# Optimization experiments

Measured on AMD Instinct MI355X. Metric: run time of the kernel, lower is better.

## Reference

```python
import jax, jax.numpy as jnp
import numpy as np

B, T, H, K, C, U, IN = 128, 800, 512, 10, 80, 64, 3


def setup_inputs() -> dict:
    key = jax.random.key(0)
    ks = jax.random.split(key, 6)
    s = 0.08  # small init so exp() window params stay stable
    return {
        "strokes": jax.random.normal(ks[0], (B, T, IN), jnp.float32),
        "sentences": jax.random.randint(ks[1], (B, U), 0, C),
        "sentences_mask": jnp.ones((B, U), jnp.float32),
        "W_ih": jax.random.normal(ks[2], (4 * H, IN + C), jnp.float32) * s,
        "W_hh": jax.random.normal(ks[3], (4 * H, H), jnp.float32) * s,
        "b_ih": jnp.zeros((4 * H,), jnp.float32),
        "b_hh": jnp.zeros((4 * H,), jnp.float32),
        "W_win": jax.random.normal(ks[4], (3 * K, H), jnp.float32) * s,
        "b_win": jnp.zeros((3 * K,), jnp.float32),
    }


def reference(strokes, sentences, sentences_mask, W_ih, W_hh, b_ih, b_hh, W_win, b_win):
    # Pre-mask the one-hot character encoding: [B, U, C]
    onehot = jax.nn.one_hot(sentences, C, dtype=jnp.float32) * sentences_mask[:, :, None]
    u = jnp.arange(U, dtype=jnp.float32)  # character position grid
    bias = b_ih + b_hh

    def step(carry, x_t):
        h, c, kappa_prev, window = carry
        inp = jnp.concatenate([x_t, window], axis=-1)           # [B, IN+C]
        gates = inp @ W_ih.T + h @ W_hh.T + bias                 # [B, 4H]
        i, f, g, o = jnp.split(gates, 4, axis=-1)                # torch LSTMCell order i,f,g,o
        i, f, o = jax.nn.sigmoid(i), jax.nn.sigmoid(f), jax.nn.sigmoid(o)
        c = f * c + i * jnp.tanh(g)
        h = o * jnp.tanh(c)
        # Gaussian window parameters (eq. 48-51 in Graves 2013)
        p = h @ W_win.T + b_win                                  # [B, 3K]
        a_hat, b_hat, k_hat = jnp.split(p, 3, axis=-1)
        alpha = jnp.exp(a_hat)
        beta = jnp.exp(b_hat)
        kappa = kappa_prev + jnp.exp(k_hat)
        # phi[b,u] = sum_k alpha * exp(-beta * (kappa - u)^2)
        d = kappa[:, :, None] - u[None, None, :]                 # [B, K, U]
        phi = jnp.sum(alpha[:, :, None] * jnp.exp(-beta[:, :, None] * d * d), axis=1)  # [B, U]
        window = jnp.einsum('bu,buc->bc', phi, onehot)           # [B, C]
        return (h, c, kappa, window), (h, window, phi)

    init = (
        jnp.zeros((B, H), jnp.float32),
        jnp.zeros((B, H), jnp.float32),
        jnp.zeros((B, K), jnp.float32),
        jnp.zeros((B, C), jnp.float32),
    )
    xs = jnp.swapaxes(strokes, 0, 1)                             # [T, B, IN]
    _, (h_seq, w_seq, phi_seq) = jax.lax.scan(step, init, xs)
    return (
        jnp.swapaxes(h_seq, 0, 1),    # [B, T, H]
        jnp.swapaxes(w_seq, 0, 1),    # [B, T, C]
        jnp.swapaxes(phi_seq, 0, 1),  # [B, T, U]
    )
```

## Files before the change

### kernel.cpp

```cpp
#include <hip/hip_runtime.h>
#include <hip/hip_bf16.h>
#include <math.h>

#define B_   128
#define T_   800
#define H_   512
#define K_   10
#define C_   80
#define U_   64
#define IN_  3

#define NG   4
#define BPG  64
#define BT   32
#define NT   256
#define KROW 608

#define WS_GPP_F (2*B_*KROW)
#define WS_BAR_F (WS_GPP_F + NG*BPG*BT*30)
#define WS_TOTAL_F (WS_BAR_F + NG*8*32)

#define OFF_H    0ull
#define OFF_W    ((size_t)B_ * T_ * H_)
#define OFF_PHI  (OFF_W + (size_t)B_ * T_ * C_)

typedef __attribute__((ext_vector_type(8))) short short8;
typedef __attribute__((ext_vector_type(4))) float f32x4;

#define SWZB(row)    (((row) ^ ((row) >> 2)) & 3)
#define SWIDX(row,k) ((row)*KROW + ((((k) >> 3) ^ SWZB(row)) << 3) + ((k) & 7))
#define LDFRAG(arr,row,u) (*(const short8*)&(arr)[(row)*KROW + (((u) ^ SWZB(row)) << 3)])

__device__ __forceinline__ void stb_f32(float* p, float v) {
  asm volatile("global_store_dword %0, %1, off sc0 sc1" :: "v"(p), "v"(v) : "memory");
}
__device__ __forceinline__ void stb_u32(unsigned* p, unsigned v) {
  asm volatile("global_store_dword %0, %1, off sc0 sc1" :: "v"(p), "v"(v) : "memory");
}
__device__ __forceinline__ void fence_vm() {
  asm volatile("s_waitcnt vmcnt(0)" ::: "memory");
}
__device__ __forceinline__ void flag_add(unsigned* p) {
  __hip_atomic_fetch_add(p, 1u, __ATOMIC_RELAXED, __HIP_MEMORY_SCOPE_AGENT);
}
__device__ __forceinline__ unsigned flag_sum(unsigned* base, int nlines) {
  unsigned s = 0;
  for (int i = 0; i < nlines; ++i)
    s += __hip_atomic_load(base + i * 32, __ATOMIC_RELAXED, __HIP_MEMORY_SCOPE_AGENT);
  return s;
}
__device__ __forceinline__ void acq_fence(unsigned* p) {
  (void)__hip_atomic_load(p, __ATOMIC_ACQUIRE, __HIP_MEMORY_SCOPE_AGENT);
}
__device__ __forceinline__ float sigmoidf_(float v) { return 1.0f / (1.0f + expf(-v)); }
__device__ __forceinline__ unsigned pack_hl(float v) {
  unsigned hb = __float_as_uint(v) >> 16;
  float rs = v - __uint_as_float(hb << 16);
  unsigned lb = __float_as_uint(rs) >> 16;
  return (hb << 16) | lb;
}

__global__ void __launch_bounds__(256, 2)
init_ws_kernel(float* __restrict__ ws) {
  size_t i = (size_t)blockIdx.x * 256 + threadIdx.x;
  const size_t n = (size_t)WS_TOTAL_F;
  const size_t stride = (size_t)gridDim.x * 256;
  for (; i < n; i += stride) ws[i] = 0.0f;
}

__global__ void __launch_bounds__(NT, 1)
graves_kernel(const float* __restrict__ x,
              const int*   __restrict__ sent,
              const float* __restrict__ smask,
              const float* __restrict__ W_ih,
              const float* __restrict__ W_hh,
              const float* __restrict__ b_ih,
              const float* __restrict__ b_hh,
              const float* __restrict__ W_win,
              const float* __restrict__ b_win,
              float* __restrict__ out,
              float* __restrict__ ws)
{
  const int tid = threadIdx.x;
  const int bid = blockIdx.x;
  const int g   = bid >> 6;
  const int ub  = bid & (BPG - 1);
  const int b0  = g * BT;
  const int u0  = ub * 8;

  unsigned* gbufu = (unsigned*)ws;
  float*    gpp   = ws + WS_GPP_F;
  unsigned* fb    = (unsigned*)(ws + WS_BAR_F) + (size_t)g * 256;
  unsigned* c1l   = fb;
  unsigned* c2l   = fb + 4 * 32;

  __shared__ __align__(16) short whi[32 * KROW];
  __shared__ __align__(16) short wlo[32 * KROW];
  __shared__ __align__(16) short shi[32 * KROW];
  __shared__ __align__(16) short slo[32 * KROW];
  __shared__ __align__(16) float glf[1024];
  __shared__ float hT[8 * 32];
  __shared__ float wwin[8 * 30];
  __shared__ float xwb[32 * 4];
  __shared__ int   sentl[U_];
  __shared__ float maskl[U_];
  __shared__ float kapl[K_ + 6];

  float* pred  = glf;
  float* pl    = glf + 256;
  float* abkA  = glf + 288;
  float* abkB  = glf + 304;
  float* abkK  = glf + 320;
  float* phim  = glf + 336;

  for (int idx = tid; idx < 32 * KROW; idx += NT) {
    const int r = idx / KROW, k = idx - r * KROW;
    const int uu = r >> 2, gate = r & 3, gr = gate * H_ + u0 + uu;
    float wv = 0.0f;
    if (k < H_)      wv = W_hh[(size_t)gr * H_ + k];
    else if (k < H_ + C_) wv = W_ih[(size_t)gr * (IN_ + C_) + IN_ + (k - H_)];
    const unsigned hb = __float_as_uint(wv) >> 16;
    const float rs = wv - __uint_as_float(hb << 16);
    const unsigned lb = __float_as_uint(rs) >> 16;
    const int li = SWIDX(r, k);
    whi[li] = (short)hb;
    wlo[li] = (short)lb;
  }
  for (int idx = tid; idx < 32 * 16; idx += NT) {
    const int b2 = idx >> 4, k = (H_ + C_) + (idx & 15);
    shi[SWIDX(b2, k)] = 0; slo[SWIDX(b2, k)] = 0;
  }
  if (tid < 32) {
    const int uu = tid >> 2, gate = tid & 3, gr = gate * H_ + u0 + uu;
    xwb[tid * 4 + 0] = W_ih[(size_t)gr * (IN_ + C_) + 0];
    xwb[tid * 4 + 1] = W_ih[(size_t)gr * (IN_ + C_) + 1];
    xwb[tid * 4 + 2] = W_ih[(size_t)gr * (IN_ + C_) + 2];
    xwb[tid * 4 + 3] = b_ih[gr] + b_hh[gr];
  }
  for (int idx = tid; idx < 240; idx += NT) {
    const int uu = idx / 30, j = idx - uu * 30;
    wwin[idx] = W_win[(size_t)j * H_ + u0 + uu];
  }
  const bool isWB = (ub < BT);
  const int  wb_b = b0 + ub;
  if (isWB) {
    if (tid < U_) { sentl[tid] = sent[wb_b * U_ + tid]; maskl[tid] = smask[wb_b * U_ + tid]; }
    if (tid < K_) kapl[tid] = 0.0f;
  }
  __syncthreads();

  const int lane = tid & 63;
  const int wid  = tid >> 6;
  const int ni   = wid & 1;
  const int kh   = wid >> 1;
  const int r16  = lane & 15;
  const int g4   = lane >> 4;
  const int bb   = ni * 16 + r16;

  float cr0 = 0.0f, cr1 = 0.0f;

#define GSTEP(ks) { \
    const int uu_ = (ks) * 4 + g4; \
    const short8 bh = LDFRAG(shi, bb, uu_); \
    const short8 bl = LDFRAG(slo, bb, uu_); \
    const short8 ah0 = LDFRAG(whi, r16, uu_); \
    const short8 al0 = LDFRAG(wlo, r16, uu_); \
    const short8 ah1 = LDFRAG(whi, 16 + r16, uu_); \
    const short8 al1 = LDFRAG(wlo, 16 + r16, uu_); \
    a0 = __builtin_amdgcn_mfma_f32_16x16x32_bf16(ah0, bh, a0, 0, 0, 0); \
    a0 = __builtin_amdgcn_mfma_f32_16x16x32_bf16(ah0, bl, a0, 0, 0, 0); \
    a0 = __builtin_amdgcn_mfma_f32_16x16x32_bf16(al0, bh, a0, 0, 0, 0); \
    a1 = __builtin_amdgcn_mfma_f32_16x16x32_bf16(ah1, bh, a1, 0, 0, 0); \
    a1 = __builtin_amdgcn_mfma_f32_16x16x32_bf16(ah1, bl, a1, 0, 0, 0); \
    a1 = __builtin_amdgcn_mfma_f32_16x16x32_bf16(al1, bh, a1, 0, 0, 0); \
  }

  for (int t = 0; t <= T_; ++t) {
    if (!isWB && t == T_) break;

    const unsigned* pIn  = gbufu + (size_t)((t & 1) ^ 1) * (B_ * KROW);
    unsigned*       pInW = gbufu + (size_t)((t & 1) ^ 1) * (B_ * KROW);
    unsigned*       pOut = gbufu + (size_t)(t & 1) * (B_ * KROW);

    if (tid == 0 && t > 0) {
      const unsigned tgt = 64u * (unsigned)t;
      while (flag_sum(c1l, 4) < tgt) __builtin_amdgcn_s_sleep(1);
      acq_fence(c1l);
    }
    __syncthreads();

    float xv0 = 0.f, xv1 = 0.f, xv2 = 0.f;
    float pv0=0,pv1=0,pv2=0,pv3=0,pv4=0,pv5=0,pv6=0,pv7=0;
    if (t < T_) {
      const int sb = tid & 31, seg = tid >> 5;
      const unsigned* grow = pIn + (size_t)(b0 + sb) * KROW + seg * 64;
      uint4 v[16];
      #pragma unroll
      for (int i = 0; i < 16; ++i) v[i] = *(const uint4*)(grow + i * 4);
      #pragma unroll
      for (int i = 0; i < 16; ++i) {
        const int k = seg * 64 + i * 4;
        const int idx = SWIDX(sb, k);
        const unsigned h01 = (v[i].x >> 16) | ((v[i].y >> 16) << 16);
        const unsigned h23 = (v[i].z >> 16) | ((v[i].w >> 16) << 16);
        const unsigned l01 = (v[i].x & 0xffffu) | ((v[i].y & 0xffffu) << 16);
        const unsigned l23 = (v[i].z & 0xffffu) | ((v[i].w & 0xffffu) << 16);
        *(uint2*)&shi[idx] = make_uint2(h01, h23);
        *(uint2*)&slo[idx] = make_uint2(l01, l23);
      }
      if (kh == 0) {
        const float* xp = x + ((size_t)(b0 + bb) * T_ + t) * IN_;
        xv0 = xp[0]; xv1 = xp[1]; xv2 = xp[2];
      }
    }
    if (isWB && t >= 1 && tid < 240) {
      const int j = tid % 30, ch = tid / 30;
      const float* gp = gpp + (((size_t)(g * BPG + ch * 8) * BT + ub) * 30 + j);
      pv0 = gp[0*BT*30]; pv1 = gp[1*BT*30]; pv2 = gp[2*BT*30]; pv3 = gp[3*BT*30];
      pv4 = gp[4*BT*30]; pv5 = gp[5*BT*30]; pv6 = gp[6*BT*30]; pv7 = gp[7*BT*30];
    }
    __syncthreads();

    if (isWB && t >= 1) {
      if (tid < 240) pred[tid] = ((pv0+pv1)+(pv2+pv3))+((pv4+pv5)+(pv6+pv7));
      __syncthreads();
      if (tid < 30) {
        float s = b_win[tid];
        #pragma unroll
        for (int ch = 0; ch < 8; ++ch) s += pred[ch * 30 + tid];
        pl[tid] = s;
      }
      __syncthreads();
      if (tid < K_) {
        abkA[tid] = expf(pl[tid]);
        abkB[tid] = expf(pl[K_ + tid]);
        const float kv = kapl[tid] + expf(pl[2 * K_ + tid]);
        kapl[tid] = kv;
        abkK[tid] = kv;
      }
      __syncthreads();
      if (tid < U_) {
        const float fu = (float)tid;
        float s = 0.0f;
        #pragma unroll
        for (int j2 = 0; j2 < K_; ++j2) {
          const float d = abkK[j2] - fu;
          s = fmaf(abkA[j2], expf(-abkB[j2] * d * d), s);
        }
        phim[tid] = s * maskl[tid];
        out[OFF_PHI + ((size_t)wb_b * T_ + (t - 1)) * U_ + tid] = s;
      }
      __syncthreads();
      if (tid < C_) {
        float wv = 0.0f;
        #pragma unroll
        for (int u = 0; u < U_; ++u) wv += (sentl[u] == tid) ? phim[u] : 0.0f;
        stb_u32(&pInW[(size_t)wb_b * KROW + H_ + tid], pack_hl(wv));
        out[OFF_W + ((size_t)wb_b * T_ + (t - 1)) * C_ + tid] = wv;
      }
      fence_vm();
      __syncthreads();
      if (tid == 0) flag_add(c2l + (ub & 1) * 32);
    }
    if (t == T_) break;

    f32x4 a0 = {0.f, 0.f, 0.f, 0.f}, a1 = {0.f, 0.f, 0.f, 0.f};
    for (int ks = kh * 8; ks < kh * 8 + 8; ++ks) GSTEP(ks);

    if (tid == 0 && t > 0) {
      const unsigned tgt = 32u * (unsigned)t;
      while (flag_sum(c2l, 2) < tgt) __builtin_amdgcn_s_sleep(1);
      acq_fence(c2l);
    }
    __syncthreads();

    {
      const int sb = tid & 31, seg = tid >> 5;
      #pragma unroll
      for (int i = 0; i < 10; ++i) {
        const int c = seg * 10 + i;
        const unsigned v = pIn[(size_t)(b0 + sb) * KROW + H_ + c];
        const int idx = SWIDX(sb, H_ + c);
        shi[idx] = (short)(v >> 16);
        slo[idx] = (short)(v & 0xffffu);
      }
    }
    __syncthreads();

    if (kh == 0) { GSTEP(16); }
    else         { GSTEP(17); GSTEP(18); }

    if (kh == 1) {
      #pragma unroll
      for (int e = 0; e < 4; ++e) {
        glf[(ni * 2 + 0) * 256 + (g4 * 4 + e) * 16 + r16] = a0[e];
        glf[(ni * 2 + 1) * 256 + (g4 * 4 + e) * 16 + r16] = a1[e];
      }
    }
    __syncthreads();
    if (kh == 0) {
      #pragma unroll
      for (int mi = 0; mi < 2; ++mi) {
        float ge[4];
        #pragma unroll
        for (int e = 0; e < 4; ++e) {
          const int r = mi * 16 + g4 * 4 + e;
          const float av = ((mi == 0) ? a0[e] : a1[e]) + glf[(ni * 2 + mi) * 256 + (g4 * 4 + e) * 16 + r16];
          ge[e] = av + xwb[r*4+0]*xv0 + xwb[r*4+1]*xv1 + xwb[r*4+2]*xv2 + xwb[r*4+3];
        }
        const float iv = sigmoidf_(ge[0]);
        const float fv = sigmoidf_(ge[1]);
        const float gv = tanhf(ge[2]);
        const float ov = sigmoidf_(ge[3]);
        const float cprev = (mi == 0) ? cr0 : cr1;
        const float cv = fmaf(fv, cprev, iv * gv);
        if (mi == 0) cr0 = cv; else cr1 = cv;
        const float hv = ov * tanhf(cv);
        const int uu = mi * 4 + g4;
        hT[uu * 32 + bb] = hv;
        stb_u32(&pOut[(size_t)(b0 + bb) * KROW + (u0 + uu)], pack_hl(hv));
        out[OFF_H + ((size_t)(b0 + bb) * T_ + t) * H_ + (u0 + uu)] = hv;
      }
    }
    __syncthreads();

    for (int it = tid; it < BT * 30; it += NT) {
      const int b2 = it / 30, j = it - b2 * 30;
      float s = 0.0f;
      #pragma unroll
      for (int uu = 0; uu < 8; ++uu) s = fmaf(wwin[uu * 30 + j], hT[uu * 32 + b2], s);
      stb_f32(&gpp[((size_t)bid * BT + b2) * 30 + j], s);
    }
    fence_vm();
    __syncthreads();
    if (tid == 0) flag_add(c1l + (ub & 3) * 32);
  }
#undef GSTEP
}

extern "C" void kernel_launch(void* const* d_in, const int* in_sizes, int n_in,
                              void* d_out, int out_size, void* d_ws, size_t ws_size,
                              hipStream_t stream) {
  const float* x     = (const float*)d_in[0];
  const int*   sent  = (const int*)  d_in[1];
  const float* smask = (const float*)d_in[2];
  const float* W_ih  = (const float*)d_in[3];
  const float* W_hh  = (const float*)d_in[4];
  const float* b_ih  = (const float*)d_in[5];
  const float* b_hh  = (const float*)d_in[6];
  const float* W_win = (const float*)d_in[7];
  const float* b_win = (const float*)d_in[8];
  float* ws  = (float*)d_ws;
  float* out = (float*)d_out;

  hipLaunchKernelGGL(init_ws_kernel, dim3(512), dim3(256), 0, stream, ws);
  hipLaunchKernelGGL(graves_kernel, dim3(NG * BPG), dim3(NT), 0, stream,
                     x, sent, smask, W_ih, W_hh, b_ih, b_hh, W_win, b_win, out, ws);
}
```

Baseline: 10.54 ms.

## Replace two-barrier window stage with atomic fixed-point accumulation and redundant per-block window compute

Instead of writer blocks gathering per-block window-projection partials and publishing the window vector behind a second grid barrier, every block atomically adds fixed-point deltas of its partial projection into a shared 64-bit accumulator. Every block then recomputes alpha, beta, kappa, phi and the window for its whole batch group locally in shared memory. This removes the second cross-block barrier and the window round trip through global memory each timestep. The cost is redundant exp work in all blocks, 64-bit atomics with fixed-point quantisation (up to about 2^-32 per partial), and __expf approximations, so results may differ slightly from before.

```diff
diff --git a/kernel.cpp b/kernel.cpp
--- a/kernel.cpp
+++ b/kernel.cpp
@@ -15,9 +15,10 @@
 #define BT   32
 #define NT   256
 #define KROW 608
-
-#define WS_GPP_F (2*B_*KROW)
-#define WS_BAR_F (WS_GPP_F + NG*BPG*BT*30)
+#define HB   512
+
+#define WS_PACC_F  (2*B_*HB)
+#define WS_BAR_F   (WS_PACC_F + NG*BT*30*2)
 #define WS_TOTAL_F (WS_BAR_F + NG*8*32)
 
 #define OFF_H    0ull
@@ -31,9 +32,6 @@
 #define SWIDX(row,k) ((row)*KROW + ((((k) >> 3) ^ SWZB(row)) << 3) + ((k) & 7))
 #define LDFRAG(arr,row,u) (*(const short8*)&(arr)[(row)*KROW + (((u) ^ SWZB(row)) << 3)])
 
-__device__ __forceinline__ void stb_f32(float* p, float v) {
-  asm volatile("global_store_dword %0, %1, off sc0 sc1" :: "v"(p), "v"(v) : "memory");
-}
 __device__ __forceinline__ void stb_u32(unsigned* p, unsigned v) {
   asm volatile("global_store_dword %0, %1, off sc0 sc1" :: "v"(p), "v"(v) : "memory");
 }
@@ -43,11 +41,8 @@
 __device__ __forceinline__ void flag_add(unsigned* p) {
   __hip_atomic_fetch_add(p, 1u, __ATOMIC_RELAXED, __HIP_MEMORY_SCOPE_AGENT);
 }
-__device__ __forceinline__ unsigned flag_sum(unsigned* base, int nlines) {
-  unsigned s = 0;
-  for (int i = 0; i < nlines; ++i)
-    s += __hip_atomic_load(base + i * 32, __ATOMIC_RELAXED, __HIP_MEMORY_SCOPE_AGENT);
-  return s;
+__device__ __forceinline__ unsigned flag_ld(unsigned* p) {
+  return __hip_atomic_load(p, __ATOMIC_RELAXED, __HIP_MEMORY_SCOPE_AGENT);
 }
 __device__ __forceinline__ void acq_fence(unsigned* p) {
   (void)__hip_atomic_load(p, __ATOMIC_ACQUIRE, __HIP_MEMORY_SCOPE_AGENT);
@@ -58,6 +53,10 @@
   float rs = v - __uint_as_float(hb << 16);
   unsigned lb = __float_as_uint(rs) >> 16;
   return (hb << 16) | lb;
+}
+__device__ __forceinline__ float comb_hl(short h, short l) {
+  return __uint_as_float((unsigned)(unsigned short)h << 16) +
+         __uint_as_float((unsigned)(unsigned short)l << 16);
 }
 
 __global__ void __launch_bounds__(256, 2)
@@ -88,36 +87,26 @@
   const int b0  = g * BT;
   const int u0  = ub * 8;
 
-  unsigned* gbufu = (unsigned*)ws;
-  float*    gpp   = ws + WS_GPP_F;
-  unsigned* fb    = (unsigned*)(ws + WS_BAR_F) + (size_t)g * 256;
-  unsigned* c1l   = fb;
-  unsigned* c2l   = fb + 4 * 32;
+  unsigned*  gbuf   = (unsigned*)ws;
+  long long* pacc_g = (long long*)(ws + WS_PACC_F) + (size_t)g * (BT * 30);
+  unsigned*  fb     = (unsigned*)(ws + WS_BAR_F) + (size_t)g * 256;
+  unsigned*  c1l    = fb;
 
   __shared__ __align__(16) short whi[32 * KROW];
   __shared__ __align__(16) short wlo[32 * KROW];
   __shared__ __align__(16) short shi[32 * KROW];
   __shared__ __align__(16) short slo[32 * KROW];
-  __shared__ __align__(16) float glf[1024];
+  __shared__ float pbufS[32][32];
   __shared__ float hT[8 * 32];
   __shared__ float wwin[8 * 30];
   __shared__ float xwb[32 * 4];
-  __shared__ int   sentl[U_];
-  __shared__ float maskl[U_];
-  __shared__ float kapl[K_ + 6];
-
-  float* pred  = glf;
-  float* pl    = glf + 256;
-  float* abkA  = glf + 288;
-  float* abkB  = glf + 304;
-  float* abkK  = glf + 320;
-  float* phim  = glf + 336;
+  float* pbf = &pbufS[0][0];
 
   for (int idx = tid; idx < 32 * KROW; idx += NT) {
     const int r = idx / KROW, k = idx - r * KROW;
     const int uu = r >> 2, gate = r & 3, gr = gate * H_ + u0 + uu;
     float wv = 0.0f;
-    if (k < H_)      wv = W_hh[(size_t)gr * H_ + k];
+    if (k < H_)           wv = W_hh[(size_t)gr * H_ + k];
     else if (k < H_ + C_) wv = W_ih[(size_t)gr * (IN_ + C_) + IN_ + (k - H_)];
     const unsigned hb = __float_as_uint(wv) >> 16;
     const float rs = wv - __uint_as_float(hb << 16);
@@ -141,13 +130,6 @@
     const int uu = idx / 30, j = idx - uu * 30;
     wwin[idx] = W_win[(size_t)j * H_ + u0 + uu];
   }
-  const bool isWB = (ub < BT);
-  const int  wb_b = b0 + ub;
-  if (isWB) {
-    if (tid < U_) { sentl[tid] = sent[wb_b * U_ + tid]; maskl[tid] = smask[wb_b * U_ + tid]; }
-    if (tid < K_) kapl[tid] = 0.0f;
-  }
-  __syncthreads();
 
   const int lane = tid & 63;
   const int wid  = tid >> 6;
@@ -157,7 +139,20 @@
   const int g4   = lane >> 4;
   const int bb   = ni * 16 + r16;
 
+  const int pb = tid >> 3, ug = tid & 7;
+  float msk[8]; int snt[8];
+  #pragma unroll
+  for (int i = 0; i < 8; ++i) {
+    msk[i] = smask[(size_t)(b0 + pb) * U_ + ug * 8 + i];
+    snt[i] = sent [(size_t)(b0 + pb) * U_ + ug * 8 + i];
+  }
+  const bool isWriter = (ub < BT);
+  const int  wb_b = b0 + ub;
+  __syncthreads();
+
   float cr0 = 0.0f, cr1 = 0.0f;
+  long long prevp[4] = {0, 0, 0, 0};
+  float kprevf[4] = {0.f, 0.f, 0.f, 0.f};
 
 #define GSTEP(ks) { \
     const int uu_ = (ks) * 4 + g4; \
@@ -176,24 +171,23 @@
   }
 
   for (int t = 0; t <= T_; ++t) {
-    if (!isWB && t == T_) break;
-
-    const unsigned* pIn  = gbufu + (size_t)((t & 1) ^ 1) * (B_ * KROW);
-    unsigned*       pInW = gbufu + (size_t)((t & 1) ^ 1) * (B_ * KROW);
-    unsigned*       pOut = gbufu + (size_t)(t & 1) * (B_ * KROW);
-
-    if (tid == 0 && t > 0) {
-      const unsigned tgt = 64u * (unsigned)t;
-      while (flag_sum(c1l, 4) < tgt) __builtin_amdgcn_s_sleep(1);
-      acq_fence(c1l);
+    if (t == T_ && !isWriter) break;
+
+    const unsigned* pIn  = gbuf + (size_t)((t & 1) ^ 1) * (B_ * HB);
+    unsigned*       pOut = gbuf + (size_t)(t & 1) * (B_ * HB);
+
+    if (t > 0 && tid < 4) {
+      unsigned* line = c1l + tid * 32;
+      const unsigned tgt = 16u * (unsigned)t;
+      while (flag_ld(line) < tgt) __builtin_amdgcn_s_sleep(1);
+      acq_fence(line);
     }
     __syncthreads();
 
     float xv0 = 0.f, xv1 = 0.f, xv2 = 0.f;
-    float pv0=0,pv1=0,pv2=0,pv3=0,pv4=0,pv5=0,pv6=0,pv7=0;
-    if (t < T_) {
+    {
       const int sb = tid & 31, seg = tid >> 5;
-      const unsigned* grow = pIn + (size_t)(b0 + sb) * KROW + seg * 64;
+      const unsigned* grow = pIn + (size_t)(b0 + sb) * HB + seg * 64;
       uint4 v[16];
       #pragma unroll
       for (int i = 0; i < 16; ++i) v[i] = *(const uint4*)(grow + i * 4);
@@ -208,93 +202,102 @@
         *(uint2*)&shi[idx] = make_uint2(h01, h23);
         *(uint2*)&slo[idx] = make_uint2(l01, l23);
       }
-      if (kh == 0) {
+      #pragma unroll
+      for (int i = 0; i < 10; ++i) {
+        const int c = seg * 10 + i;
+        const int idx = SWIDX(sb, H_ + c);
+        shi[idx] = 0; slo[idx] = 0;
+      }
+      if (kh == 0 && t < T_) {
         const float* xp = x + ((size_t)(b0 + bb) * T_ + t) * IN_;
         xv0 = xp[0]; xv1 = xp[1]; xv2 = xp[2];
       }
     }
-    if (isWB && t >= 1 && tid < 240) {
-      const int j = tid % 30, ch = tid / 30;
-      const float* gp = gpp + (((size_t)(g * BPG + ch * 8) * BT + ub) * 30 + j);
-      pv0 = gp[0*BT*30]; pv1 = gp[1*BT*30]; pv2 = gp[2*BT*30]; pv3 = gp[3*BT*30];
-      pv4 = gp[4*BT*30]; pv5 = gp[5*BT*30]; pv6 = gp[6*BT*30]; pv7 = gp[7*BT*30];
-    }
-    __syncthreads();
-
-    if (isWB && t >= 1) {
-      if (tid < 240) pred[tid] = ((pv0+pv1)+(pv2+pv3))+((pv4+pv5)+(pv6+pv7));
+    __syncthreads();
+
+    if (t >= 1) {
+      #pragma unroll
+      for (int r = 0; r < 4; ++r) {
+        const int item = tid + 256 * r;
+        if (item < 960) {
+          const int b = item / 30, j = item - b * 30;
+          const long long v = pacc_g[b * 30 + j];
+          const int hi = (int)(v >> 32);
+          const unsigned lo = (unsigned)(v & 0xffffffffLL);
+          const float pv = (float)hi + (float)lo * 0x1p-32f + b_win[j];
+          float ev = __expf(pv);
+          if (j >= 20) { ev += kprevf[r]; kprevf[r] = ev; }
+          pbufS[b][j] = ev;
+        }
+      }
       __syncthreads();
-      if (tid < 30) {
-        float s = b_win[tid];
-        #pragma unroll
-        for (int ch = 0; ch < 8; ++ch) s += pred[ch * 30 + tid];
-        pl[tid] = s;
-      }
-      __syncthreads();
-      if (tid < K_) {
-        abkA[tid] = expf(pl[tid]);
-        abkB[tid] = expf(pl[K_ + tid]);
-        const float kv = kapl[tid] + expf(pl[2 * K_ + tid]);
-        kapl[tid] = kv;
-        abkK[tid] = kv;
-      }
-      __syncthreads();
-      if (tid < U_) {
-        const float fu = (float)tid;
+
+      float al[10], be[10], ka[10];
+      #pragma unroll
+      for (int k2 = 0; k2 < 10; ++k2) {
+        al[k2] = pbufS[pb][k2];
+        be[k2] = pbufS[pb][10 + k2];
+        ka[k2] = pbufS[pb][20 + k2];
+      }
+      float ph[8];
+      #pragma unroll
+      for (int i = 0; i < 8; ++i) {
+        const float fu = (float)(ug * 8 + i);
         float s = 0.0f;
         #pragma unroll
-        for (int j2 = 0; j2 < K_; ++j2) {
-          const float d = abkK[j2] - fu;
-          s = fmaf(abkA[j2], expf(-abkB[j2] * d * d), s);
+        for (int k2 = 0; k2 < 10; ++k2) {
+          const float d = ka[k2] - fu;
+          s = fmaf(al[k2], __expf(-be[k2] * d * d), s);
         }
-        phim[tid] = s * maskl[tid];
-        out[OFF_PHI + ((size_t)wb_b * T_ + (t - 1)) * U_ + tid] = s;
+        ph[i] = s;
+      }
+      if (isWriter && pb == ub) {
+        #pragma unroll
+        for (int i = 0; i < 8; ++i)
+          out[OFF_PHI + ((size_t)wb_b * T_ + (t - 1)) * U_ + ug * 8 + i] = ph[i];
+      }
+      #pragma unroll
+      for (int i = 0; i < 8; ++i) ph[i] *= msk[i];
+
+      #pragma unroll
+      for (int r = 0; r < 8; ++r) {
+        if (ug == r) {
+          #pragma unroll
+          for (int i = 0; i < 8; ++i) {
+            const int idx = SWIDX(pb, H_ + snt[i]);
+            float cur = comb_hl(shi[idx], slo[idx]) + ph[i];
+            const unsigned pk = pack_hl(cur);
+            shi[idx] = (short)(pk >> 16);
+            slo[idx] = (short)(pk & 0xffffu);
+          }
+        }
+        asm volatile("" ::: "memory");
       }
       __syncthreads();
-      if (tid < C_) {
-        float wv = 0.0f;
-        #pragma unroll
-        for (int u = 0; u < U_; ++u) wv += (sentl[u] == tid) ? phim[u] : 0.0f;
-        stb_u32(&pInW[(size_t)wb_b * KROW + H_ + tid], pack_hl(wv));
-        out[OFF_W + ((size_t)wb_b * T_ + (t - 1)) * C_ + tid] = wv;
-      }
-      fence_vm();
-      __syncthreads();
-      if (tid == 0) flag_add(c2l + (ub & 1) * 32);
+      if (isWriter && tid < C_) {
+        const int idx = SWIDX(ub, H_ + tid);
+        out[OFF_W + ((size_t)wb_b * T_ + (t - 1)) * C_ + tid] = comb_hl(shi[idx], slo[idx]);
+      }
     }
     if (t == T_) break;
 
     f32x4 a0 = {0.f, 0.f, 0.f, 0.f}, a1 = {0.f, 0.f, 0.f, 0.f};
-    for (int ks = kh * 8; ks < kh * 8 + 8; ++ks) GSTEP(ks);
-
-    if (tid == 0 && t > 0) {
-      const unsigned tgt = 32u * (unsigned)t;
-      while (flag_sum(c2l, 2) < tgt) __builtin_amdgcn_s_sleep(1);
-      acq_fence(c2l);
-    }
-    __syncthreads();
-
-    {
-      const int sb = tid & 31, seg = tid >> 5;
-      #pragma unroll
-      for (int i = 0; i < 10; ++i) {
-        const int c = seg * 10 + i;
-        const unsigned v = pIn[(size_t)(b0 + sb) * KROW + H_ + c];
-        const int idx = SWIDX(sb, H_ + c);
-        shi[idx] = (short)(v >> 16);
-        slo[idx] = (short)(v & 0xffffu);
-      }
-    }
-    __syncthreads();
-
-    if (kh == 0) { GSTEP(16); }
-    else         { GSTEP(17); GSTEP(18); }
-
+    if (kh == 0) {
+      #pragma unroll
+      for (int ks = 0; ks < 8; ++ks) GSTEP(ks);
+      GSTEP(16);
+    } else {
+      #pragma unroll
+      for (int ks = 8; ks < 16; ++ks) GSTEP(ks);
+      GSTEP(17); GSTEP(18);
+    }
+
+    __syncthreads();
     if (kh == 1) {
       #pragma unroll
       for (int e = 0; e < 4; ++e) {
-        glf[(ni * 2 + 0) * 256 + (g4 * 4 + e) * 16 + r16] = a0[e];
-        glf[(ni * 2 + 1) * 256 + (g4 * 4 + e) * 16 + r16] = a1[e];
+        pbf[(ni * 2 + 0) * 256 + (g4 * 4 + e) * 16 + r16] = a0[e];
+        pbf[(ni * 2 + 1) * 256 + (g4 * 4 + e) * 16 + r16] = a1[e];
       }
     }
     __syncthreads();
@@ -305,7 +308,7 @@
         #pragma unroll
         for (int e = 0; e < 4; ++e) {
           const int r = mi * 16 + g4 * 4 + e;
-          const float av = ((mi == 0) ? a0[e] : a1[e]) + glf[(ni * 2 + mi) * 256 + (g4 * 4 + e) * 16 + r16];
+          const float av = ((mi == 0) ? a0[e] : a1[e]) + pbf[(ni * 2 + mi) * 256 + (g4 * 4 + e) * 16 + r16];
           ge[e] = av + xwb[r*4+0]*xv0 + xwb[r*4+1]*xv1 + xwb[r*4+2]*xv2 + xwb[r*4+3];
         }
         const float iv = sigmoidf_(ge[0]);
@@ -318,18 +321,26 @@
         const float hv = ov * tanhf(cv);
         const int uu = mi * 4 + g4;
         hT[uu * 32 + bb] = hv;
-        stb_u32(&pOut[(size_t)(b0 + bb) * KROW + (u0 + uu)], pack_hl(hv));
+        stb_u32(&pOut[(size_t)(b0 + bb) * HB + (u0 + uu)], pack_hl(hv));
         out[OFF_H + ((size_t)(b0 + bb) * T_ + t) * H_ + (u0 + uu)] = hv;
       }
     }
     __syncthreads();
 
-    for (int it = tid; it < BT * 30; it += NT) {
-      const int b2 = it / 30, j = it - b2 * 30;
-      float s = 0.0f;
-      #pragma unroll
-      for (int uu = 0; uu < 8; ++uu) s = fmaf(wwin[uu * 30 + j], hT[uu * 32 + b2], s);
-      stb_f32(&gpp[((size_t)bid * BT + b2) * 30 + j], s);
+    #pragma unroll
+    for (int r = 0; r < 4; ++r) {
+      const int item = tid + 256 * r;
+      if (item < 960) {
+        const int b = item / 30, j = item - b * 30;
+        float s = 0.0f;
+        #pragma unroll
+        for (int uu = 0; uu < 8; ++uu) s = fmaf(wwin[uu * 30 + j], hT[uu * 32 + b], s);
+        const long long nv = llrintf(s * 4294967296.0f);
+        const unsigned long long d = (unsigned long long)(nv - prevp[r]);
+        prevp[r] = nv;
+        __hip_atomic_fetch_add((unsigned long long*)(pacc_g + b * 30 + j), d,
+                               __ATOMIC_RELAXED, __HIP_MEMORY_SCOPE_AGENT);
+      }
     }
     fence_vm();
     __syncthreads();
```

New measurement: 11.77 ms. 11.6% more time.
